# Optimization experiments

Measured on AMD Instinct MI355X. Metric: run time of the kernel, lower is better.

Reference implementation:

```python
import jax, jax.numpy as jnp
import numpy as np

B, H, W, C = 32, 56, 56, 384
NH, WS, SS = 12, 7, 3
HD = C // NH
HID = 4 * C
N = WS * WS
NW = (H // WS) * (W // WS)


def _rel_pos_index():
    coords = np.stack(np.meshgrid(np.arange(WS), np.arange(WS), indexing='ij')).reshape(2, -1)
    rel = (coords[:, :, None] - coords[:, None, :]).transpose(1, 2, 0)
    rel[..., 0] += WS - 1
    rel[..., 1] += WS - 1
    rel[..., 0] *= 2 * WS - 1
    return rel.sum(-1)  # (N, N) int


def _shift_mask():
    img = np.zeros((H, W))
    cnt = 0
    sl = (slice(0, -WS), slice(-WS, -SS), slice(-SS, None))
    for hs in sl:
        for ws_ in sl:
            img[hs, ws_] = cnt
            cnt += 1
    mw = img.reshape(H // WS, WS, W // WS, WS).transpose(0, 2, 1, 3).reshape(-1, N)
    diff = mw[:, None, :] - mw[:, :, None]  # (nW, N, N)
    return np.where(diff != 0, -100.0, 0.0).astype(np.float32)


_REL_IDX = _rel_pos_index()
_MASK = _shift_mask()


def _ln(x, g, b, eps=1e-5):
    m = jnp.mean(x, -1, keepdims=True)
    v = jnp.mean(jnp.square(x - m), -1, keepdims=True)
    return (x - m) * jax.lax.rsqrt(v + eps) * g + b


def setup_inputs() -> dict:
    key = jax.random.key(0)
    ks = jax.random.split(key, 8)
    s = 0.02
    return {
        'x': jax.random.normal(ks[0], (B, H * W, C), jnp.float32),
        'ln1_g': jnp.ones((C,)), 'ln1_b': jnp.zeros((C,)),
        'qkv_w': jax.random.normal(ks[1], (C, 3 * C)) * s, 'qkv_b': jnp.zeros((3 * C,)),
        'rel_bias': jax.random.normal(ks[2], ((2 * WS - 1) ** 2, NH)) * s,
        'proj_w': jax.random.normal(ks[3], (C, C)) * s, 'proj_b': jnp.zeros((C,)),
        'ln2_g': jnp.ones((C,)), 'ln2_b': jnp.zeros((C,)),
        'fc1_w': jax.random.normal(ks[4], (C, HID)) * s, 'fc1_b': jnp.zeros((HID,)),
        'fc2_w': jax.random.normal(ks[5], (HID, C)) * s, 'fc2_b': jnp.zeros((C,)),
    }


def _forward(x, ln1_g, ln1_b, qkv_w, qkv_b, rel_bias, proj_w, proj_b,
             ln2_g, ln2_b, fc1_w, fc1_b, fc2_w, fc2_b):
    mask = jnp.asarray(_MASK)
    shortcut = x
    y = _ln(x, ln1_g, ln1_b).reshape(B, H, W, C)
    y = jnp.roll(y, (-SS, -SS), axis=(1, 2))
    # window partition -> (B*nW, N, C)
    y = y.reshape(B, H // WS, WS, W // WS, WS, C).transpose(0, 1, 3, 2, 4, 5)
    win = y.reshape(-1, N, C)
    Bn = win.shape[0]
    qkv = (win @ qkv_w + qkv_b).reshape(Bn, N, 3, NH, HD).transpose(2, 0, 3, 1, 4)
    q, k, v = qkv[0] * (HD ** -0.5), qkv[1], qkv[2]  # (Bn, NH, N, HD)
    attn = jnp.einsum('whid,whjd->whij', q, k)
    bias = rel_bias[_REL_IDX.reshape(-1)].reshape(N, N, NH).transpose(2, 0, 1)
    attn = attn + bias[None]
    attn = attn.reshape(B, NW, NH, N, N) + mask[None, :, None]
    attn = jax.nn.softmax(attn.reshape(Bn, NH, N, N), axis=-1)
    out = jnp.einsum('whij,whjd->whid', attn, v).transpose(0, 2, 1, 3).reshape(Bn, N, C)
    out = out @ proj_w + proj_b
    # window reverse + roll back
    out = out.reshape(B, H // WS, W // WS, WS, WS, C).transpose(0, 1, 3, 2, 4, 5).reshape(B, H, W, C)
    out = jnp.roll(out, (SS, SS), axis=(1, 2)).reshape(B, H * W, C)
    x = shortcut + out
    h = jax.nn.gelu(_ln(x, ln2_g, ln2_b) @ fc1_w + fc1_b, approximate=False)
    ffn = jax.nn.gelu(h @ fc2_w + fc2_b, approximate=False)  # repo MLP has act after 2nd linear
    return x + ffn


def reference(x, ln1_g, ln1_b, qkv_w, qkv_b, rel_bias, proj_w, proj_b,
              ln2_g, ln2_b, fc1_w, fc1_b, fc2_w, fc2_b):
    return _forward(x, ln1_g, ln1_b, qkv_w, qkv_b, rel_bias, proj_w, proj_b,
                    ln2_g, ln2_b, fc1_w, fc1_b, fc2_w, fc2_b)
```

## Files before the change

kernel.cpp:

```cpp
#include <hip/hip_runtime.h>
#include <hip/hip_bf16.h>
#include <cstdint>
#include <cstddef>


typedef __attribute__((ext_vector_type(8))) short bf16x8;
typedef __attribute__((ext_vector_type(4))) float f32x4;

__device__ __forceinline__ float bf2f(__hip_bfloat16 x) { return __bfloat162float(x); }
__device__ __forceinline__ __hip_bfloat16 f2bf(float x) { return __float2bfloat16(x); }
__device__ __forceinline__ float s2f(short s) {
    unsigned u = ((unsigned)(unsigned short)s) << 16;
    return __builtin_bit_cast(float, u);
}
__device__ __forceinline__ short f2s(float f) {
    __hip_bfloat16 h = __float2bfloat16(f);
    return (short)__builtin_bit_cast(unsigned short, h);
}
__device__ __forceinline__ float gelu_exact(float x) {
    return 0.5f * x * (1.0f + erff(x * 0.70710678118654752f));
}

__global__ __launch_bounds__(256)
void ln_stats_bf16(const __hip_bfloat16* __restrict__ src, float* __restrict__ stats)
{
    int t = blockIdx.x * 4 + (threadIdx.x >> 6);
    int lane = threadIdx.x & 63;
    const __hip_bfloat16* p = src + (size_t)t * 384 + lane * 6;
    float s = 0.f, s2 = 0.f;
#pragma unroll
    for (int u = 0; u < 6; ++u) { float f = bf2f(p[u]); s += f; s2 += f * f; }
#pragma unroll
    for (int off = 32; off > 0; off >>= 1) { s += __shfl_xor(s, off); s2 += __shfl_xor(s2, off); }
    if (lane == 0) {
        float mean = s * (1.f / 384.f);
        float var  = fmaxf(s2 * (1.f / 384.f) - mean * mean, 0.f);
        stats[2 * t]     = mean;
        stats[2 * t + 1] = rsqrtf(var + 1e-5f);
    }
}

__global__ __launch_bounds__(256)
void wconv_kernel(const float* __restrict__ W, __hip_bfloat16* __restrict__ Wt,
                  int K, int N, int total)
{
    int idx = blockIdx.x * 256 + threadIdx.x;
    if (idx >= total) return;
    int k = idx / N, n = idx - k * N;
    Wt[(size_t)n * K + k] = f2bf(W[idx]);
}

__global__ __launch_bounds__(256)
void ln1_gather_kernel(const float* __restrict__ x,
                       const float* __restrict__ g,
                       const float* __restrict__ bb,
                       __hip_bfloat16* __restrict__ wbuf)
{
    int wrow = blockIdx.x * 4 + (threadIdx.x >> 6);
    int lane = threadIdx.x & 63;
    int bi = wrow / 49, n = wrow - bi * 49;
    int b_ = bi >> 6, wid = bi & 63;
    int wh = wid >> 3, ww = wid & 7;
    int r = n / 7, c = n - (n / 7) * 7;
    int sh = wh * 7 + r + 3; if (sh >= 56) sh -= 56;
    int sw = ww * 7 + c + 3; if (sw >= 56) sw -= 56;
    const float* p = x + (size_t)(b_ * 3136 + sh * 56 + sw) * 384 + lane * 6;
    float v[6];
    float2 v01 = *(const float2*)p;
    float2 v23 = *(const float2*)(p + 2);
    float2 v45 = *(const float2*)(p + 4);
    v[0] = v01.x; v[1] = v01.y; v[2] = v23.x; v[3] = v23.y; v[4] = v45.x; v[5] = v45.y;
    float s = 0.f, s2 = 0.f;
#pragma unroll
    for (int u = 0; u < 6; ++u) { s += v[u]; s2 += v[u] * v[u]; }
#pragma unroll
    for (int off = 32; off > 0; off >>= 1) { s += __shfl_xor(s, off); s2 += __shfl_xor(s2, off); }
    float mean = s * (1.f / 384.f);
    float var  = fmaxf(s2 * (1.f / 384.f) - mean * mean, 0.f);
    float rstd = rsqrtf(var + 1e-5f);
    __hip_bfloat16* dst = wbuf + (size_t)wrow * 384 + lane * 6;
#pragma unroll
    for (int u = 0; u < 6; ++u) {
        int ch = lane * 6 + u;
        dst[u] = f2bf((v[u] - mean) * rstd * g[ch] + bb[ch]);
    }
}

__global__ __launch_bounds__(256)
void attn_kernel(const __hip_bfloat16* __restrict__ qkv,
                 const float* __restrict__ rel_bias,
                 __hip_bfloat16* __restrict__ attn_out,
                 int win_base)
{
    const int wi = blockIdx.x / 12;
    const int nh = blockIdx.x - wi * 12;
    const int gwin = win_base + wi;
    const int wid = gwin & 63;
    const int wh = wid >> 3, ww = wid & 7;
    const int tid = threadIdx.x;

    __shared__ alignas(16) float sQ[49 * 36];
    __shared__ alignas(16) float sK[49 * 36];
    __shared__ alignas(16) float sV[49 * 36];
    __shared__ float sS[49 * 49];
    __shared__ float sBias[169];
    __shared__ unsigned char sGrp[49];

    for (int idx = tid; idx < 169; idx += 256) sBias[idx] = rel_bias[idx * 12 + nh];
    if (tid < 49) {
        int r = tid / 7, c = tid - (tid / 7) * 7;
        int gh = (wh == 7) ? ((r < 4) ? 1 : 2) : 0;
        int gw = (ww == 7) ? ((c < 4) ? 1 : 2) : 0;
        sGrp[tid] = (unsigned char)(gh * 3 + gw);
    }
    for (int s = tid; s < 588; s += 256) {
        int which = s / 196, rem = s - which * 196;
        int row = rem >> 2, seg = rem & 3;
        bf16x8 vv = *(const bf16x8*)(qkv + (size_t)(wi * 49 + row) * 1152
                                     + which * 384 + nh * 32 + seg * 8);
        float* dstp = (which == 0 ? sQ : which == 1 ? sK : sV) + row * 36 + seg * 8;
#pragma unroll
        for (int e = 0; e < 8; ++e) dstp[e] = s2f(vv[e]);
    }
    __syncthreads();

    for (int idx = tid; idx < 2401; idx += 256) {
        int i = idx / 49, j = idx - (idx / 49) * 49;
        const float* qp = sQ + i * 36;
        const float* kp = sK + j * 36;
        float acc = 0.f;
#pragma unroll
        for (int d = 0; d < 32; ++d) acc += qp[d] * kp[d];
        int ri = i / 7, ci = i - (i / 7) * 7;
        int rj = j / 7, cj = j - (j / 7) * 7;
        float bias = sBias[(ri - rj + 6) * 13 + (ci - cj + 6)];
        float msk = (sGrp[i] == sGrp[j]) ? 0.f : -100.f;
        sS[idx] = acc * 0.17677669529663689f + bias + msk;
    }
    __syncthreads();

    if (tid < 196) {
        int i = tid >> 2, l4 = tid & 3;
        float mx = -1e30f;
        for (int j = l4; j < 49; j += 4) mx = fmaxf(mx, sS[i * 49 + j]);
        mx = fmaxf(mx, __shfl_xor(mx, 1, 4));
        mx = fmaxf(mx, __shfl_xor(mx, 2, 4));
        float sum = 0.f;
        for (int j = l4; j < 49; j += 4) {
            float e = expf(sS[i * 49 + j] - mx);
            sS[i * 49 + j] = e; sum += e;
        }
        sum += __shfl_xor(sum, 1, 4);
        sum += __shfl_xor(sum, 2, 4);
        float inv = 1.f / sum;
        for (int j = l4; j < 49; j += 4) sS[i * 49 + j] *= inv;
    }
    __syncthreads();

    __hip_bfloat16* dst = attn_out + (size_t)gwin * 49 * 384 + nh * 32;
    for (int idx = tid; idx < 1568; idx += 256) {
        int i = idx >> 5, d = idx & 31;
        const float* sp = sS + i * 49;
        float acc = 0.f;
#pragma unroll
        for (int j = 0; j < 49; ++j) acc += sp[j] * sV[j * 36 + d];
        dst[(size_t)i * 384 + d] = f2bf(acc);
    }
}

template<int MODE>
__global__ __launch_bounds__(256)
void gemm_mfma(const __hip_bfloat16* __restrict__ A,
               const __hip_bfloat16* __restrict__ Bt,
               const float* __restrict__ bias,
               const float* __restrict__ x_in,
               const float* __restrict__ lnst,
               const float* __restrict__ ln_g,
               const float* __restrict__ ln_b,
               const __hip_bfloat16* __restrict__ res,
               __hip_bfloat16* __restrict__ out_h,
               float* __restrict__ out_f,
               int N, int K, int m_base)
{
    __shared__ alignas(16) __hip_bfloat16 As[128 * 40];
    __shared__ alignas(16) __hip_bfloat16 Bs[128 * 40];
    const int tid = threadIdx.x;
    const int bm = blockIdx.y, bn = blockIdx.x;
    const int lane = tid & 63;
    const int w = tid >> 6, wr = w >> 1, wc = w & 1;
    const int fr = lane & 15, fq = lane >> 4;

    f32x4 acc[4][4] = {};

    const int r0 = tid >> 2, ks0 = tid & 3;
    const int r1 = r0 + 64;
    const __hip_bfloat16* Aptr0 = A + (size_t)(bm * 128 + r0) * K + ks0 * 8;
    const __hip_bfloat16* Aptr1 = A + (size_t)(bm * 128 + r1) * K + ks0 * 8;
    const __hip_bfloat16* Bptr0 = Bt + (size_t)(bn * 128 + r0) * K + ks0 * 8;
    const __hip_bfloat16* Bptr1 = Bt + (size_t)(bn * 128 + r1) * K + ks0 * 8;

    float lm0 = 0.f, lr0 = 0.f, lm1 = 0.f, lr1 = 0.f;
    if (MODE == 1) {
        lm0 = lnst[2 * (bm * 128 + r0)]; lr0 = lnst[2 * (bm * 128 + r0) + 1];
        lm1 = lnst[2 * (bm * 128 + r1)]; lr1 = lnst[2 * (bm * 128 + r1) + 1];
    }

    for (int kk = 0; kk < K; kk += 32) {
        bf16x8 a0 = *(const bf16x8*)(Aptr0 + kk);
        bf16x8 a1 = *(const bf16x8*)(Aptr1 + kk);
        bf16x8 b0 = *(const bf16x8*)(Bptr0 + kk);
        bf16x8 b1 = *(const bf16x8*)(Bptr1 + kk);
        if (MODE == 1) {
            float4 g0 = *(const float4*)(ln_g + kk + ks0 * 8);
            float4 g1 = *(const float4*)(ln_g + kk + ks0 * 8 + 4);
            float4 c0 = *(const float4*)(ln_b + kk + ks0 * 8);
            float4 c1 = *(const float4*)(ln_b + kk + ks0 * 8 + 4);
            float gv[8] = {g0.x, g0.y, g0.z, g0.w, g1.x, g1.y, g1.z, g1.w};
            float cv[8] = {c0.x, c0.y, c0.z, c0.w, c1.x, c1.y, c1.z, c1.w};
#pragma unroll
            for (int e = 0; e < 8; ++e) {
                a0[e] = f2s((s2f(a0[e]) - lm0) * lr0 * gv[e] + cv[e]);
                a1[e] = f2s((s2f(a1[e]) - lm1) * lr1 * gv[e] + cv[e]);
            }
        }
        __syncthreads();
        *(bf16x8*)&As[r0 * 40 + ks0 * 8] = a0;
        *(bf16x8*)&As[r1 * 40 + ks0 * 8] = a1;
        *(bf16x8*)&Bs[r0 * 40 + ks0 * 8] = b0;
        *(bf16x8*)&Bs[r1 * 40 + ks0 * 8] = b1;
        __syncthreads();
        bf16x8 af[4], bfv[4];
#pragma unroll
        for (int mi = 0; mi < 4; ++mi)
            af[mi] = *(const bf16x8*)&As[(wr * 64 + mi * 16 + fr) * 40 + fq * 8];
#pragma unroll
        for (int ni = 0; ni < 4; ++ni)
            bfv[ni] = *(const bf16x8*)&Bs[(wc * 64 + ni * 16 + fr) * 40 + fq * 8];
#pragma unroll
        for (int mi = 0; mi < 4; ++mi)
#pragma unroll
            for (int ni = 0; ni < 4; ++ni)
                acc[mi][ni] = __builtin_amdgcn_mfma_f32_16x16x32_bf16(
                    af[mi], bfv[ni], acc[mi][ni], 0, 0, 0);
    }

    const int mrow0 = bm * 128 + wr * 64;
    const int ncol0 = bn * 128 + wc * 64;
    float bias_v[4];
#pragma unroll
    for (int ni = 0; ni < 4; ++ni) bias_v[ni] = bias[ncol0 + ni * 16 + fr];

#pragma unroll
    for (int mi = 0; mi < 4; ++mi) {
#pragma unroll
        for (int r = 0; r < 4; ++r) {
            int m = mrow0 + mi * 16 + fq * 4 + r;
            if (MODE == 0) {
                int biw = m / 49, n_ = m - biw * 49;
                int b_ = biw >> 6, wid = biw & 63;
                int wh = wid >> 3, ww = wid & 7;
                int rr = n_ / 7, cc = n_ - (n_ / 7) * 7;
                int h = wh * 7 + rr + 3; if (h >= 56) h -= 56;
                int wcol = ww * 7 + cc + 3; if (wcol >= 56) wcol -= 56;
                size_t drow = (size_t)(b_ * 3136 + h * 56 + wcol) * 384;
#pragma unroll
                for (int ni = 0; ni < 4; ++ni) {
                    int nc = ncol0 + ni * 16 + fr;
                    float v = acc[mi][ni][r] + bias_v[ni];
                    out_h[drow + nc] = f2bf(x_in[drow + nc] + v);
                }
            } else if (MODE == 1) {
                size_t o = (size_t)m * N;
#pragma unroll
                for (int ni = 0; ni < 4; ++ni) {
                    int nc = ncol0 + ni * 16 + fr;
                    out_h[o + nc] = f2bf(gelu_exact(acc[mi][ni][r] + bias_v[ni]));
                }
            } else if (MODE == 2) {
                size_t og = (size_t)(m_base + m) * 384;
                size_t ol = (size_t)m * 384;
#pragma unroll
                for (int ni = 0; ni < 4; ++ni) {
                    int nc = ncol0 + ni * 16 + fr;
                    out_f[og + nc] = bf2f(res[ol + nc])
                                   + gelu_exact(acc[mi][ni][r] + bias_v[ni]);
                }
            } else {
                size_t o = (size_t)m * N;
#pragma unroll
                for (int ni = 0; ni < 4; ++ni) {
                    int nc = ncol0 + ni * 16 + fr;
                    out_h[o + nc] = f2bf(acc[mi][ni][r] + bias_v[ni]);
                }
            }
        }
    }
}

extern "C" void kernel_launch(void* const* d_in, const int* in_sizes, int n_in,
                              void* d_out, int out_size, void* d_ws, size_t ws_size,
                              hipStream_t stream)
{
    (void)in_sizes; (void)n_in; (void)out_size; (void)ws_size;
    const float* x      = (const float*)d_in[0];
    const float* ln1_g  = (const float*)d_in[1];
    const float* ln1_b  = (const float*)d_in[2];
    const float* qkv_w  = (const float*)d_in[3];
    const float* qkv_b  = (const float*)d_in[4];
    const float* rel_b  = (const float*)d_in[5];
    const float* proj_w = (const float*)d_in[6];
    const float* proj_b = (const float*)d_in[7];
    const float* ln2_g  = (const float*)d_in[8];
    const float* ln2_b  = (const float*)d_in[9];
    const float* fc1_w  = (const float*)d_in[10];
    const float* fc1_b  = (const float*)d_in[11];
    const float* fc2_w  = (const float*)d_in[12];
    const float* fc2_b  = (const float*)d_in[13];
    float* out = (float*)d_out;

    __hip_bfloat16* aout = (__hip_bfloat16*)d_out;
    __hip_bfloat16* wbuf = (__hip_bfloat16*)((char*)d_out + 77070336);
    __hip_bfloat16* xmid = wbuf;

    char* ws = (char*)d_ws;
    float* ln2s = (float*)ws;
    __hip_bfloat16* qkv_wt  = (__hip_bfloat16*)(ws + 802816);
    __hip_bfloat16* proj_wt = (__hip_bfloat16*)(ws + 1687552);
    __hip_bfloat16* fc1_wt  = (__hip_bfloat16*)(ws + 1982464);
    __hip_bfloat16* fc2_wt  = (__hip_bfloat16*)(ws + 3162112);
    __hip_bfloat16* qkvbuf  = (__hip_bfloat16*)(ws + 4341760);
    __hip_bfloat16* hbuf    = (__hip_bfloat16*)(ws + 4341760);
    __hip_bfloat16* resb    = (__hip_bfloat16*)(ws + 4341760 + 38535168);

    wconv_kernel<<<1728, 256, 0, stream>>>(qkv_w,  qkv_wt,  384, 1152, 442368);
    wconv_kernel<<<576,  256, 0, stream>>>(proj_w, proj_wt, 384, 384,  147456);
    wconv_kernel<<<2304, 256, 0, stream>>>(fc1_w,  fc1_wt,  384, 1536, 589824);
    wconv_kernel<<<2304, 256, 0, stream>>>(fc2_w,  fc2_wt,  1536, 384, 589824);

    ln1_gather_kernel<<<25088, 256, 0, stream>>>(x, ln1_g, ln1_b, wbuf);

    for (int c = 0; c < 8; ++c) {
        size_t mb = (size_t)c * 12544;
        gemm_mfma<3><<<dim3(9, 98), 256, 0, stream>>>(
            wbuf + mb * 384, qkv_wt, qkv_b, nullptr, nullptr, nullptr, nullptr, nullptr,
            qkvbuf, nullptr, 1152, 384, 0);
        attn_kernel<<<3072, 256, 0, stream>>>(qkvbuf, rel_b, aout, c * 256);
    }

    gemm_mfma<0><<<dim3(3, 784), 256, 0, stream>>>(
        aout, proj_wt, proj_b, x, nullptr, nullptr, nullptr, nullptr,
        xmid, nullptr, 384, 384, 0);

    ln_stats_bf16<<<25088, 256, 0, stream>>>(xmid, ln2s);

    for (int c = 0; c < 8; ++c) {
        size_t mb = (size_t)c * 12544;
        gemm_mfma<1><<<dim3(12, 98), 256, 0, stream>>>(
            xmid + mb * 384, fc1_wt, fc1_b, nullptr, ln2s + 2 * mb, ln2_g, ln2_b, nullptr,
            hbuf, nullptr, 1536, 384, 0);
        if (c < 7) {
            gemm_mfma<2><<<dim3(3, 98), 256, 0, stream>>>(
                hbuf, fc2_wt, fc2_b, nullptr, nullptr, nullptr, nullptr,
                xmid + mb * 384, nullptr, out, 384, 1536, (int)mb);
        } else {
            hipMemcpyAsync(resb, xmid + (size_t)94080 * 384, (size_t)6272 * 384 * 2,
                           hipMemcpyDeviceToDevice, stream);
            gemm_mfma<2><<<dim3(3, 49), 256, 0, stream>>>(
                hbuf, fc2_wt, fc2_b, nullptr, nullptr, nullptr, nullptr,
                xmid + (size_t)87808 * 384, nullptr, out, 384, 1536, 87808);
            gemm_mfma<2><<<dim3(3, 49), 256, 0, stream>>>(
                hbuf + (size_t)6272 * 1536, fc2_wt, fc2_b, nullptr, nullptr, nullptr, nullptr,
                resb, nullptr, out, 384, 1536, 94080);
        }
    }
}
```

Before: 1.827 ms.

## Stage GEMM epilogue through LDS for vector stores and remap blocks per XCD

For the plain and GELU GEMM modes, the accumulator tile is written to shared memory that aliases the A/B staging buffers. It is then stored to global memory as 16-byte vectors, replacing scattered 2-byte stores. Block IDs are also remapped so that consecutive tiles land on the same XCD, which should improve L2 reuse of shared A/B panels. This adds two barriers and a larger shared allocation that may lower occupancy.

```diff
diff --git a/kernel.cpp b/kernel.cpp
--- a/kernel.cpp
+++ b/kernel.cpp
@@ -182,10 +182,21 @@
                float* __restrict__ out_f,
                int N, int K, int m_base)
 {
-    __shared__ alignas(16) __hip_bfloat16 As[128 * 40];
-    __shared__ alignas(16) __hip_bfloat16 Bs[128 * 40];
+    __shared__ alignas(16) char smem[128 * 136 * 2];
+    __hip_bfloat16* As = (__hip_bfloat16*)smem;
+    __hip_bfloat16* Bs = (__hip_bfloat16*)(smem + 10240);
+    __hip_bfloat16* Cs = (__hip_bfloat16*)smem;
+
     const int tid = threadIdx.x;
-    const int bm = blockIdx.y, bn = blockIdx.x;
+
+    const int nwg = gridDim.x * gridDim.y;
+    int orig = blockIdx.y * gridDim.x + blockIdx.x;
+    int q = nwg >> 3, r = nwg & 7;
+    int xcd = orig & 7, pos = orig >> 3;
+    int id = xcd * q + ((xcd < r) ? xcd : r) + pos;
+    const int bm = id / gridDim.x;
+    const int bn = id - bm * gridDim.x;
+
     const int lane = tid & 63;
     const int w = tid >> 6, wr = w >> 1, wc = w & 1;
     const int fr = lane & 15, fq = lane >> 4;
@@ -250,47 +261,57 @@
 #pragma unroll
     for (int ni = 0; ni < 4; ++ni) bias_v[ni] = bias[ncol0 + ni * 16 + fr];
 
+    if (MODE == 1 || MODE == 3) {
+        __syncthreads();
+#pragma unroll
+        for (int mi = 0; mi < 4; ++mi)
+#pragma unroll
+            for (int rr = 0; rr < 4; ++rr) {
+                int row = wr * 64 + mi * 16 + fq * 4 + rr;
+#pragma unroll
+                for (int ni = 0; ni < 4; ++ni) {
+                    int col = wc * 64 + ni * 16 + fr;
+                    float v = acc[mi][ni][rr] + bias_v[ni];
+                    Cs[row * 136 + col] = f2bf(MODE == 1 ? gelu_exact(v) : v);
+                }
+            }
+        __syncthreads();
+        int row = tid >> 1, half = tid & 1;
+        size_t o = (size_t)(bm * 128 + row) * N + bn * 128 + half * 64;
+        const __hip_bfloat16* src = &Cs[row * 136 + half * 64];
+#pragma unroll
+        for (int j = 0; j < 8; ++j)
+            *(bf16x8*)(out_h + o + j * 8) = *(const bf16x8*)(src + j * 8);
+        return;
+    }
+
 #pragma unroll
     for (int mi = 0; mi < 4; ++mi) {
 #pragma unroll
-        for (int r = 0; r < 4; ++r) {
-            int m = mrow0 + mi * 16 + fq * 4 + r;
+        for (int rr = 0; rr < 4; ++rr) {
+            int m = mrow0 + mi * 16 + fq * 4 + rr;
             if (MODE == 0) {
                 int biw = m / 49, n_ = m - biw * 49;
                 int b_ = biw >> 6, wid = biw & 63;
                 int wh = wid >> 3, ww = wid & 7;
-                int rr = n_ / 7, cc = n_ - (n_ / 7) * 7;
-                int h = wh * 7 + rr + 3; if (h >= 56) h -= 56;
+                int rw = n_ / 7, cc = n_ - (n_ / 7) * 7;
+                int h = wh * 7 + rw + 3; if (h >= 56) h -= 56;
                 int wcol = ww * 7 + cc + 3; if (wcol >= 56) wcol -= 56;
                 size_t drow = (size_t)(b_ * 3136 + h * 56 + wcol) * 384;
 #pragma unroll
                 for (int ni = 0; ni < 4; ++ni) {
                     int nc = ncol0 + ni * 16 + fr;
-                    float v = acc[mi][ni][r] + bias_v[ni];
+                    float v = acc[mi][ni][rr] + bias_v[ni];
                     out_h[drow + nc] = f2bf(x_in[drow + nc] + v);
                 }
-            } else if (MODE == 1) {
-                size_t o = (size_t)m * N;
-#pragma unroll
-                for (int ni = 0; ni < 4; ++ni) {
-                    int nc = ncol0 + ni * 16 + fr;
-                    out_h[o + nc] = f2bf(gelu_exact(acc[mi][ni][r] + bias_v[ni]));
-                }
-            } else if (MODE == 2) {
+            } else {
                 size_t og = (size_t)(m_base + m) * 384;
                 size_t ol = (size_t)m * 384;
 #pragma unroll
                 for (int ni = 0; ni < 4; ++ni) {
                     int nc = ncol0 + ni * 16 + fr;
                     out_f[og + nc] = bf2f(res[ol + nc])
-                                   + gelu_exact(acc[mi][ni][r] + bias_v[ni]);
-                }
-            } else {
-                size_t o = (size_t)m * N;
-#pragma unroll
-                for (int ni = 0; ni < 4; ++ni) {
-                    int nc = ncol0 + ni * 16 + fr;
-                    out_h[o + nc] = f2bf(acc[mi][ni][r] + bias_v[ni]);
+                                   + gelu_exact(acc[mi][ni][rr] + bias_v[ni]);
                 }
             }
         }
```

After: 1.869 ms. +2.3%, slower.
